# Performance work log

Measured on AMD Instinct MI355X. Metric: run time of the kernel, lower is better.

The kernel has to match this reference:

```python
import jax, jax.numpy as jnp
import numpy as np

N_HIDDEN = 512
BATCH = 16
MAX_LEN = 4096


def setup_inputs() -> dict:
    key = jax.random.key(0)
    k1, k2, k3 = jax.random.split(key, 3)
    h = jax.random.normal(k1, (BATCH, N_HIDDEN, MAX_LEN), dtype=jnp.float32)
    # Conv1d weight [out_ch=3*nh, in_ch=nh, kernel=2], fan-in scaled
    W = jax.random.normal(k2, (3 * N_HIDDEN, N_HIDDEN, 2), dtype=jnp.float32) / np.float32(np.sqrt(2.0 * N_HIDDEN))
    b = 0.02 * jax.random.normal(k3, (3 * N_HIDDEN,), dtype=jnp.float32)
    b = b.at[2 * N_HIDDEN:].set(1.0)  # init_gate_bias on the gate third of the bias
    # lengths: grouped (unique_consecutive) and sorted descending, padded into width MAX_LEN
    N = jnp.array([4096] * 4 + [3000] * 4 + [2048] * 4 + [1000] * 4, dtype=jnp.int32)
    return {"h": h, "W": W, "b": b, "N": N}


def _conv_reduce(h, W, b):
    # _reduce: Conv1d(nh -> 3*nh, kernel=2, stride=2) then gated combine (dropout=0).
    B, C, L = h.shape
    Lp = L + (L % 2)
    x = jnp.pad(h, ((0, 0), (0, 0), (0, Lp - L))).reshape(B, C, Lp // 2, 2)
    lrg = jnp.einsum('bclk,ock->bol', x, W) + b[None, :, None]  # [B, 3C, L//2]
    l = lrg[:, :C]
    r = jnp.tanh(lrg[:, C:2 * C])
    g = jax.nn.sigmoid(lrg[:, 2 * C:])
    return l * g + r * (1.0 - g)


def _forward(h, W, b, N):
    B, nh, L = h.shape
    # Nfp2 = largest power of two <= N ; M = 2*(N - Nfp2)
    Nfp2 = (2 ** jnp.floor(jnp.log2(N.astype(jnp.float32)))).astype(N.dtype)
    M = 2 * (N - Nfp2)
    # --- prefix reduce + suffix cat (padded/masked equivalent of _suffix_cat) ---
    # conv is local (k=2, s=2), so reducing the full padded width gives identical
    # values at the kept positions j < M//2.
    red = _conv_reduce(h, W, b)                      # [B, nh, ceil(L/2)]
    red = jnp.pad(red, ((0, 0), (0, 0), (0, L - red.shape[-1])))
    j = jnp.arange(L)
    half = (M // 2)[:, None]                         # [B, 1]
    take_red = j[None, :] < half                     # first M//2 slots <- reduced prefix
    idx = jnp.where(take_red, j[None, :], jnp.minimum(j[None, :] + half, L - 1))
    suf = jnp.take_along_axis(h, jnp.broadcast_to(idx[:, None, :], (B, nh, L)), axis=2)
    cur = jnp.where(take_red[:, None, :], red, suf)  # per-seq length now Nfp2 (power of 2)
    n = Nfp2
    # --- halving tree reduction; freeze sequences that reached length 1 ---
    steps = int(np.floor(np.log2(L)))
    for _ in range(steps):
        red = _conv_reduce(cur, W, b)
        neww = red.shape[-1]
        active = (n > 1)[:, None, None]
        cur = jnp.where(active, red, cur[:, :, :neww])
        n = jnp.where(n > 1, n // 2, n)
    return cur[:, :, 0]  # squeeze(-1) -> [B, nh]


def reference(h, W, b, N):
    return _forward(h, W, b, N)
```

## Files before the change

### kernel.cpp

```cpp
#include <hip/hip_runtime.h>

#define BATCH 16
#define CH 512
#define OC 1536
#define KDIM 1024
#define LMAX 4096
#define WGLOB_SZ 3145728
#define CTR_OFF 76546048

typedef __attribute__((ext_vector_type(8))) _Float16 h8v;
typedef __attribute__((ext_vector_type(4))) float f4v;

__device__ __forceinline__ int nfp2_of(int n) { return 1 << (31 - __clz(n)); }

__device__ __forceinline__ unsigned short h2u(_Float16 h) {
  union { _Float16 h; unsigned short u; } v; v.h = h; return v.u;
}

__device__ __forceinline__ void layout(const int* __restrict__ Nvec, int b,
                                       size_t& offC0, size_t& offA, size_t& offB,
                                       int& n, int& nfp2, int& half) {
  size_t c0t = 0, at = 0, bt = 0, c0o = 0, ao = 0, bo = 0;
  n = 2; nfp2 = 2; half = 0;
#pragma unroll 1
  for (int i = 0; i < BATCH; ++i) {
    int ni = Nvec[i];
    int f = nfp2_of(ni);
    int hf = ni - f;
    size_t cs = (size_t)((hf + 127) & ~127) << 11;
    size_t as = (size_t)(f >> 1) << 11;
    size_t bs = (size_t)(f >> 2) << 11;
    if (i < b) { c0o += cs; ao += as; bo += bs; }
    if (i == b) { n = ni; nfp2 = f; half = hf; }
    c0t += cs; at += as; bt += bs;
  }
  offC0 = (size_t)WGLOB_SZ + c0o;
  offA = (size_t)WGLOB_SZ + c0t + ao;
  offB = (size_t)WGLOB_SZ + c0t + at + bo;
}

__device__ __forceinline__ void gload16(const void* g, void* l) {
  __builtin_amdgcn_global_load_lds((const __attribute__((address_space(1))) void*)g,
                                   (__attribute__((address_space(3))) void*)l, 16, 0, 0);
}
__device__ __forceinline__ void gload16c(const void* g, void* l) {
  __builtin_amdgcn_global_load_lds((const __attribute__((address_space(1))) void*)g,
                                   (__attribute__((address_space(3))) void*)l, 16, 0, 1);
}

__global__ __launch_bounds__(256) void prep_w_k(const float* __restrict__ W, char* __restrict__ ws) {
  int idx = blockIdx.x * 256 + threadIdx.x;
  if (idx >= 16 * 1536) return;
  int step = idx / 1536;
  int o = idx - step * 1536;
  const float* src = W + (size_t)o * KDIM + step * 64;
  unsigned short hb[64];
#pragma unroll
  for (int t = 0; t < 64; ++t) hb[t] = h2u((_Float16)src[t]);
  uint4* d4 = (uint4*)(ws + ((size_t)idx << 7));
#pragma unroll
  for (int s = 0; s < 8; ++s) {
    int oc = (s ^ (o & 7)) * 8;
    uint4 v;
    v.x = (unsigned)hb[oc + 0] | ((unsigned)hb[oc + 1] << 16);
    v.y = (unsigned)hb[oc + 2] | ((unsigned)hb[oc + 3] << 16);
    v.z = (unsigned)hb[oc + 4] | ((unsigned)hb[oc + 5] << 16);
    v.w = (unsigned)hb[oc + 6] | ((unsigned)hb[oc + 7] << 16);
    d4[s] = v;
  }
}

__global__ void init_ctr_k(char* __restrict__ ws) {
  ((unsigned*)(ws + CTR_OFF))[threadIdx.x] = 0u;
}

__global__ __launch_bounds__(256) void reorg_h_k(const float* __restrict__ h,
                                                 const int* __restrict__ Nvec,
                                                 char* __restrict__ ws,
                                                 float* __restrict__ dout, int mode) {
  __shared__ char T[32 * 256];
  const int b = blockIdx.z;
  size_t offC0, offA, offB; int n, nfp2, half;
  layout(Nvec, b, offC0, offA, offB, n, nfp2, half);
  const int tid = threadIdx.x;
  const int by = blockIdx.y;
  const int c0 = by * 64;

  if (mode == 1 && nfp2 == 1) {
    if (blockIdx.x == 0 && tid < 64)
      dout[(size_t)b * CH + c0 + tid] = h[(size_t)b * CH * LMAX + (size_t)(c0 + tid) * LMAX];
    return;
  }

  const int d0 = blockIdx.x * 32;
  int dlo, dhi, soff;
  size_t base;
  if (mode == 0) { dlo = 0; dhi = half; soff = 0; base = offC0; }
  else { dlo = half >> 1; dhi = nfp2 >> 1; soff = half; base = offA; }
  if (d0 >= dhi || d0 + 32 <= dlo) return;

  const float* hb = h + (size_t)b * CH * LMAX;

#pragma unroll
  for (int q = 0; q < 8; ++q) {
    int id = q * 256 + tid;
    int cl = id >> 5;
    int dl = id & 31;
    int d = d0 + dl;
    bool ok = (d < dhi) && (d >= dlo);
    float2 v;
    v.x = 0.f; v.y = 0.f;
    if (ok) v = *(const float2*)(hb + (size_t)(c0 + cl) * LMAX + 2 * d + soff);
    unsigned u = (unsigned)h2u((_Float16)v.x) | ((unsigned)h2u((_Float16)v.y) << 16);
    int g = cl >> 2;
    *(unsigned*)(T + dl * 256 + ((g ^ (dl & 15)) << 4) + (cl & 3) * 4) = u;
  }
  __syncthreads();
#pragma unroll
  for (int qq = 0; qq < 2; ++qq) {
    int gid = qq * 256 + tid;
    int dl = gid >> 4;
    int s = gid & 15;
    int d = d0 + dl;
    if (d >= dhi || d < dlo) continue;
    uint4 val = *(const uint4*)(T + dl * 256 + ((s ^ (dl & 15)) << 4));
    size_t dst = base + ((size_t)d << 11) + (size_t)((2 * by + (s >> 3)) << 7) +
                 (((s & 7) ^ (d & 7)) << 4);
    *(uint4*)(ws + dst) = val;
  }
}

__device__ __forceinline__ void gate_store(const f4v acc[6][4], const float* __restrict__ bias,
                                           char* outp, float* __restrict__ dout,
                                           int b, int o0, int rg, int cg, int lq, int lane15,
                                           int l0, int cols, bool fin) {
#pragma unroll
  for (int s = 0; s < 2; ++s) {
#pragma unroll
    for (int cf = 0; cf < 4; ++cf) {
      f4v vl = acc[s][cf], vr = acc[2 + s][cf], vg = acc[4 + s][cf];
      int l = l0 + cg * 64 + cf * 16 + lane15;
      if (l >= cols) continue;
      int P = l >> 1, par = l & 1;
#pragma unroll
      for (int j = 0; j < 4; ++j) {
        int c = o0 + rg * 32 + s * 16 + lq * 4 + j;
        float zl = vl[j] + bias[c];
        float zr = vr[j] + bias[CH + c];
        float zg = vg[j] + bias[2 * CH + c];
        float g = 1.f / (1.f + __expf(-zg));
        float rt = 1.f - 2.f / (1.f + __expf(2.f * zr));
        float val = zl * g + rt * (1.f - g);
        if (fin) {
          if (l == 0) dout[(size_t)b * CH + c] = val;
        } else {
          int k = 2 * c + par;
          size_t byte = ((size_t)P << 11) + (size_t)((k >> 6) << 7) +
                        ((((k >> 3) & 7) ^ (P & 7)) << 4) + ((k & 7) << 1);
          *(unsigned short*)(outp + byte) = h2u((_Float16)val);
        }
      }
    }
  }
}

__global__ __launch_bounds__(256, 2) void mfma_level_k(const float* __restrict__ bias,
                                                       const int* __restrict__ Nvec,
                                                       char* __restrict__ ws,
                                                       float* __restrict__ dout,
                                                       int level, int tiles) {
  __shared__ char smem[81920];
  const int id = blockIdx.x;
  const int o0 = (id & 7) * 64;
  const int r2 = id >> 3;
  const int xb = r2 % tiles;
  const int b = r2 / tiles;
  if (b >= BATCH) return;

  size_t offC0, offA, offB; int n, nfp2, half;
  layout(Nvec, b, offC0, offA, offB, n, nfp2, half);

  int cols;
  size_t inOff, outOff;
  if (level == 0) {
    if (half == 0) return;
    cols = half;
    inOff = offC0;
    outOff = offA;
  } else {
    int w = nfp2 >> (level - 1);
    if (w < 2) return;
    cols = w >> 1;
    if (cols <= 128) return;
    inOff = (level & 1) ? offA : offB;
    outOff = (level & 1) ? offB : offA;
  }
  const int l0 = xb * 128;
  if (l0 >= cols) return;

  const int tid = threadIdx.x;
  const int lane = tid & 63, wid = tid >> 6;
  const int lane15 = lane & 15, lq = lane >> 4;
  const int rg = wid & 1, cg = wid >> 1;
  const char* inp = ws + inOff;

  unsigned aoff[6]; int adst[6];
#pragma unroll
  for (int q = 0; q < 6; ++q) {
    int d = q * 4096 + tid * 16;
    int r = d >> 7;
    int p = d & 127;
    int o = ((r >> 6) << 9) + o0 + (r & 63);
    aoff[q] = ((unsigned)o << 7) + p;
    adst[q] = q * 4096 + wid * 1024;
  }
  unsigned boff[4]; int bdst[4];
#pragma unroll
  for (int q = 0; q < 4; ++q) {
    int d = q * 4096 + tid * 16;
    int l = d >> 7;
    int p = d & 127;
    int lc = l0 + l; if (lc > cols - 1) lc = cols - 1;
    boff[q] = ((unsigned)lc << 11) + p;
    bdst[q] = q * 4096 + wid * 1024;
  }

#define STAGE(st, sel) do {                                                  \
    char* Ab = smem + (sel) * 24576;                                         \
    char* Bb = smem + 49152 + (sel) * 16384;                                 \
    unsigned ka = (unsigned)(st) * 196608u;                                  \
    unsigned kb = (unsigned)(st) << 7;                                       \
    _Pragma("unroll") for (int q = 0; q < 6; ++q)                            \
      gload16(ws + ka + aoff[q], Ab + adst[q]);                              \
    _Pragma("unroll") for (int q = 0; q < 4; ++q)                            \
      gload16(inp + kb + boff[q], Bb + bdst[q]);                             \
  } while (0)

  f4v acc[6][4];
#pragma unroll
  for (int m = 0; m < 6; ++m)
#pragma unroll
    for (int cf = 0; cf < 4; ++cf) acc[m][cf] = (f4v){0.f, 0.f, 0.f, 0.f};

  STAGE(0, 0);
  __syncthreads();

#pragma unroll 1
  for (int st = 0; st < 16; ++st) {
    const int cur = st & 1;
    if (st + 1 < 16) STAGE(st + 1, cur ^ 1);
    const char* Asb = smem + cur * 24576;
    const char* Bsb = smem + 49152 + cur * 16384;

#pragma unroll
    for (int s2 = 0; s2 < 2; ++s2) {
      const int oct = (s2 << 2) | lq;
      h8v bh[4];
#pragma unroll
      for (int cf = 0; cf < 4; ++cf) {
        int ll = cg * 64 + cf * 16 + lane15;
        bh[cf] = *(const h8v*)(Bsb + ll * 128 + ((oct ^ (ll & 7)) << 4));
      }
#pragma unroll
      for (int m = 0; m < 6; ++m) {
        int rr = (m >> 1) * 64 + rg * 32 + (m & 1) * 16 + lane15;
        h8v ah = *(const h8v*)(Asb + rr * 128 + ((oct ^ (rr & 7)) << 4));
#pragma unroll
        for (int cf = 0; cf < 4; ++cf)
          acc[m][cf] = __builtin_amdgcn_mfma_f32_16x16x32_f16(ah, bh[cf], acc[m][cf], 0, 0, 0);
      }
    }
    __syncthreads();
  }
#undef STAGE

  bool fin = (level > 0) && ((nfp2 >> level) == 1);
  gate_store(acc, bias, ws + outOff, dout, b, o0, rg, cg, lq, lane15, l0, cols, fin);
}

__global__ __launch_bounds__(256, 2) void tail_k(const float* __restrict__ bias,
                                                 const int* __restrict__ Nvec,
                                                 char* __restrict__ ws,
                                                 float* __restrict__ dout) {
  __shared__ char smem[81920];
  const int id = blockIdx.x;
  const int b = id & 15;
  const int o0 = (id >> 4) * 64;

  size_t offC0, offA, offB; int n, nfp2, half;
  layout(Nvec, b, offC0, offA, offB, n, nfp2, half);
  if (nfp2 < 2) return;

  const int tid = threadIdx.x;
  const int lane = tid & 63, wid = tid >> 6;
  const int lane15 = lane & 15, lq = lane >> 4;
  const int rg = wid & 1, cg = wid >> 1;

  unsigned aoff[6]; int adst[6];
#pragma unroll
  for (int q = 0; q < 6; ++q) {
    int d = q * 4096 + tid * 16;
    int r = d >> 7;
    int p = d & 127;
    int o = ((r >> 6) << 9) + o0 + (r & 63);
    aoff[q] = ((unsigned)o << 7) + p;
    adst[q] = q * 4096 + wid * 1024;
  }

  unsigned* ctr = (unsigned*)(ws + CTR_OFF) + b * 16;

  int lev = 1;
  while ((nfp2 >> lev) > 128) ++lev;

#pragma unroll 1
  for (;; ++lev) {
    int w = nfp2 >> (lev - 1);
    if (w < 2) break;
    const int cols = nfp2 >> lev;
    const bool fin = (cols == 1);
    const char* inp = ws + ((lev & 1) ? offA : offB);
    char* outp = ws + ((lev & 1) ? offB : offA);

    unsigned boff[4]; int bdst[4];
#pragma unroll
    for (int q = 0; q < 4; ++q) {
      int d = q * 4096 + tid * 16;
      int l = d >> 7;
      int p = d & 127;
      int lc = l; if (lc > cols - 1) lc = cols - 1;
      boff[q] = ((unsigned)lc << 11) + p;
      bdst[q] = q * 4096 + wid * 1024;
    }

#define STAGE_T(st, sel) do {                                                \
    char* Ab = smem + (sel) * 24576;                                         \
    char* Bb = smem + 49152 + (sel) * 16384;                                 \
    unsigned ka = (unsigned)(st) * 196608u;                                  \
    unsigned kb = (unsigned)(st) << 7;                                       \
    _Pragma("unroll") for (int q = 0; q < 6; ++q)                            \
      gload16(ws + ka + aoff[q], Ab + adst[q]);                              \
    _Pragma("unroll") for (int q = 0; q < 4; ++q)                            \
      gload16c(inp + kb + boff[q], Bb + bdst[q]);                            \
  } while (0)

    f4v acc[6][4];
#pragma unroll
    for (int m = 0; m < 6; ++m)
#pragma unroll
      for (int cf = 0; cf < 4; ++cf) acc[m][cf] = (f4v){0.f, 0.f, 0.f, 0.f};

    STAGE_T(0, 0);
    __syncthreads();

#pragma unroll 1
    for (int st = 0; st < 16; ++st) {
      const int cur = st & 1;
      if (st + 1 < 16) STAGE_T(st + 1, cur ^ 1);
      const char* Asb = smem + cur * 24576;
      const char* Bsb = smem + 49152 + cur * 16384;

#pragma unroll
      for (int s2 = 0; s2 < 2; ++s2) {
        const int oct = (s2 << 2) | lq;
        h8v bh[4];
#pragma unroll
        for (int cf = 0; cf < 4; ++cf) {
          int ll = cg * 64 + cf * 16 + lane15;
          bh[cf] = *(const h8v*)(Bsb + ll * 128 + ((oct ^ (ll & 7)) << 4));
        }
#pragma unroll
        for (int m = 0; m < 6; ++m) {
          int rr = (m >> 1) * 64 + rg * 32 + (m & 1) * 16 + lane15;
          h8v ah = *(const h8v*)(Asb + rr * 128 + ((oct ^ (rr & 7)) << 4));
#pragma unroll
          for (int cf = 0; cf < 4; ++cf)
            acc[m][cf] = __builtin_amdgcn_mfma_f32_16x16x32_f16(ah, bh[cf], acc[m][cf], 0, 0, 0);
        }
      }
      __syncthreads();
    }
#undef STAGE_T

    gate_store(acc, bias, outp, dout, b, o0, rg, cg, lq, lane15, 0, cols, fin);
    if (fin) break;

    __threadfence();
    __syncthreads();
    if (tid == 0) {
      atomicAdd(ctr + lev, 1u);
      while (atomicAdd(ctr + lev, 0u) < 8u) __builtin_amdgcn_s_sleep(8);
    }
    __syncthreads();
  }
}

extern "C" void kernel_launch(void* const* d_in, const int* in_sizes, int n_in,
                              void* d_out, int out_size, void* d_ws, size_t ws_size,
                              hipStream_t stream) {
  const float* h = (const float*)d_in[0];
  const float* W = (const float*)d_in[1];
  const float* bias = (const float*)d_in[2];
  const int* Nvec = (const int*)d_in[3];
  float* dout = (float*)d_out;
  char* ws = (char*)d_ws;

  prep_w_k<<<dim3(96), 256, 0, stream>>>(W, ws);
  init_ctr_k<<<dim3(1), 256, 0, stream>>>(ws);
  reorg_h_k<<<dim3(64, 8, BATCH), 256, 0, stream>>>(h, Nvec, ws, dout, 0);
  reorg_h_k<<<dim3(64, 8, BATCH), 256, 0, stream>>>(h, Nvec, ws, dout, 1);

  mfma_level_k<<<dim3(8 * 8 * BATCH), 256, 0, stream>>>(bias, Nvec, ws, dout, 0, 8);
  for (int lev = 1; lev <= 4; ++lev) {
    int tiles = (LMAX >> lev) / 128;
    mfma_level_k<<<dim3(tiles * 8 * BATCH), 256, 0, stream>>>(bias, Nvec, ws, dout, lev, tiles);
  }
  tail_k<<<dim3(128), 256, 0, stream>>>(bias, Nvec, ws, dout);
}
```

Measured before the change: 527.3 us.

## Widen level GEMM tiles and pipeline A/B loads with triple buffering

```diff
diff --git a/kernel.cpp b/kernel.cpp
--- a/kernel.cpp
+++ b/kernel.cpp
@@ -164,12 +164,12 @@
   }
 }
 
-__global__ __launch_bounds__(256, 2) void mfma_level_k(const float* __restrict__ bias,
+__global__ __launch_bounds__(512, 2) void mfma_level_k(const float* __restrict__ bias,
                                                        const int* __restrict__ Nvec,
                                                        char* __restrict__ ws,
                                                        float* __restrict__ dout,
                                                        int level, int tiles) {
-  __shared__ char smem[81920];
+  __shared__ char smem[139264];
   const int id = blockIdx.x;
   const int o0 = (id & 7) * 64;
   const int r2 = id >> 3;
@@ -195,7 +195,7 @@
     inOff = (level & 1) ? offA : offB;
     outOff = (level & 1) ? offB : offA;
   }
-  const int l0 = xb * 128;
+  const int l0 = xb * 256;
   if (l0 >= cols) return;
 
   const int tid = threadIdx.x;
@@ -204,34 +204,36 @@
   const int rg = wid & 1, cg = wid >> 1;
   const char* inp = ws + inOff;
 
-  unsigned aoff[6]; int adst[6];
-#pragma unroll
-  for (int q = 0; q < 6; ++q) {
-    int d = q * 4096 + tid * 16;
+  unsigned aoff[3]; int adst[3];
+#pragma unroll
+  for (int q = 0; q < 3; ++q) {
+    int d = q * 8192 + tid * 16;
     int r = d >> 7;
     int p = d & 127;
     int o = ((r >> 6) << 9) + o0 + (r & 63);
     aoff[q] = ((unsigned)o << 7) + p;
-    adst[q] = q * 4096 + wid * 1024;
+    adst[q] = q * 8192 + wid * 1024;
   }
   unsigned boff[4]; int bdst[4];
 #pragma unroll
   for (int q = 0; q < 4; ++q) {
-    int d = q * 4096 + tid * 16;
+    int d = q * 8192 + tid * 16;
     int l = d >> 7;
     int p = d & 127;
     int lc = l0 + l; if (lc > cols - 1) lc = cols - 1;
     boff[q] = ((unsigned)lc << 11) + p;
-    bdst[q] = q * 4096 + wid * 1024;
-  }
-
-#define STAGE(st, sel) do {                                                  \
+    bdst[q] = q * 8192 + wid * 1024;
+  }
+
+#define STAGE_A(st, sel) do {                                                \
     char* Ab = smem + (sel) * 24576;                                         \
-    char* Bb = smem + 49152 + (sel) * 16384;                                 \
     unsigned ka = (unsigned)(st) * 196608u;                                  \
+    _Pragma("unroll") for (int q = 0; q < 3; ++q)                            \
+      gload16(ws + ka + aoff[q], Ab + adst[q]);                              \
+  } while (0)
+#define STAGE_B(st, sel) do {                                                \
+    char* Bb = smem + 73728 + (sel) * 32768;                                 \
     unsigned kb = (unsigned)(st) << 7;                                       \
-    _Pragma("unroll") for (int q = 0; q < 6; ++q)                            \
-      gload16(ws + ka + aoff[q], Ab + adst[q]);                              \
     _Pragma("unroll") for (int q = 0; q < 4; ++q)                            \
       gload16(inp + kb + boff[q], Bb + bdst[q]);                             \
   } while (0)
@@ -242,15 +244,22 @@
 #pragma unroll
     for (int cf = 0; cf < 4; ++cf) acc[m][cf] = (f4v){0.f, 0.f, 0.f, 0.f};
 
-  STAGE(0, 0);
-  __syncthreads();
-
+  STAGE_A(0, 0);
+  STAGE_B(0, 0);
+  STAGE_A(1, 1);
+
+  int acur = 0, anx2 = 2;
 #pragma unroll 1
   for (int st = 0; st < 16; ++st) {
-    const int cur = st & 1;
-    if (st + 1 < 16) STAGE(st + 1, cur ^ 1);
-    const char* Asb = smem + cur * 24576;
-    const char* Bsb = smem + 49152 + cur * 16384;
+    if (st < 15) asm volatile("s_waitcnt vmcnt(3) lgkmcnt(0)" ::: "memory");
+    else         asm volatile("s_waitcnt vmcnt(0) lgkmcnt(0)" ::: "memory");
+    __builtin_amdgcn_s_barrier();
+    asm volatile("" ::: "memory");
+    if (st + 1 < 16) STAGE_B(st + 1, (st + 1) & 1);
+    if (st + 2 < 16) STAGE_A(st + 2, anx2);
+
+    const char* Asb = smem + acur * 24576;
+    const char* Bsb = smem + 73728 + (st & 1) * 32768;
 
 #pragma unroll
     for (int s2 = 0; s2 < 2; ++s2) {
@@ -261,6 +270,7 @@
         int ll = cg * 64 + cf * 16 + lane15;
         bh[cf] = *(const h8v*)(Bsb + ll * 128 + ((oct ^ (ll & 7)) << 4));
       }
+      __builtin_amdgcn_s_setprio(1);
 #pragma unroll
       for (int m = 0; m < 6; ++m) {
         int rr = (m >> 1) * 64 + rg * 32 + (m & 1) * 16 + lane15;
@@ -269,10 +279,13 @@
         for (int cf = 0; cf < 4; ++cf)
           acc[m][cf] = __builtin_amdgcn_mfma_f32_16x16x32_f16(ah, bh[cf], acc[m][cf], 0, 0, 0);
       }
+      __builtin_amdgcn_s_setprio(0);
     }
-    __syncthreads();
-  }
-#undef STAGE
+    acur = (acur == 2) ? 0 : acur + 1;
+    anx2 = (anx2 == 2) ? 0 : anx2 + 1;
+  }
+#undef STAGE_A
+#undef STAGE_B
 
   bool fin = (level > 0) && ((nfp2 >> level) == 1);
   gate_store(acc, bias, ws + outOff, dout, b, o0, rg, cg, lq, lane15, l0, cols, fin);
@@ -282,7 +295,7 @@
                                                  const int* __restrict__ Nvec,
                                                  char* __restrict__ ws,
                                                  float* __restrict__ dout) {
-  __shared__ char smem[81920];
+  __shared__ char smem[106496];
   const int id = blockIdx.x;
   const int b = id & 15;
   const int o0 = (id >> 4) * 64;
@@ -332,13 +345,15 @@
       bdst[q] = q * 4096 + wid * 1024;
     }
 
-#define STAGE_T(st, sel) do {                                                \
+#define STAGE_AT(st, sel) do {                                               \
     char* Ab = smem + (sel) * 24576;                                         \
-    char* Bb = smem + 49152 + (sel) * 16384;                                 \
     unsigned ka = (unsigned)(st) * 196608u;                                  \
-    unsigned kb = (unsigned)(st) << 7;                                       \
     _Pragma("unroll") for (int q = 0; q < 6; ++q)                            \
       gload16(ws + ka + aoff[q], Ab + adst[q]);                              \
+  } while (0)
+#define STAGE_BT(st, sel) do {                                               \
+    char* Bb = smem + 73728 + (sel) * 16384;                                 \
+    unsigned kb = (unsigned)(st) << 7;                                       \
     _Pragma("unroll") for (int q = 0; q < 4; ++q)                            \
       gload16c(inp + kb + boff[q], Bb + bdst[q]);                            \
   } while (0)
@@ -349,15 +364,22 @@
 #pragma unroll
       for (int cf = 0; cf < 4; ++cf) acc[m][cf] = (f4v){0.f, 0.f, 0.f, 0.f};
 
-    STAGE_T(0, 0);
-    __syncthreads();
-
+    STAGE_AT(0, 0);
+    STAGE_BT(0, 0);
+    STAGE_AT(1, 1);
+
+    int acur = 0, anx2 = 2;
 #pragma unroll 1
     for (int st = 0; st < 16; ++st) {
-      const int cur = st & 1;
-      if (st + 1 < 16) STAGE_T(st + 1, cur ^ 1);
-      const char* Asb = smem + cur * 24576;
-      const char* Bsb = smem + 49152 + cur * 16384;
+      if (st < 15) asm volatile("s_waitcnt vmcnt(6) lgkmcnt(0)" ::: "memory");
+      else         asm volatile("s_waitcnt vmcnt(0) lgkmcnt(0)" ::: "memory");
+      __builtin_amdgcn_s_barrier();
+      asm volatile("" ::: "memory");
+      if (st + 1 < 16) STAGE_BT(st + 1, (st + 1) & 1);
+      if (st + 2 < 16) STAGE_AT(st + 2, anx2);
+
+      const char* Asb = smem + acur * 24576;
+      const char* Bsb = smem + 73728 + (st & 1) * 16384;
 
 #pragma unroll
       for (int s2 = 0; s2 < 2; ++s2) {
@@ -377,9 +399,11 @@
             acc[m][cf] = __builtin_amdgcn_mfma_f32_16x16x32_f16(ah, bh[cf], acc[m][cf], 0, 0, 0);
         }
       }
-      __syncthreads();
+      acur = (acur == 2) ? 0 : acur + 1;
+      anx2 = (anx2 == 2) ? 0 : anx2 + 1;
     }
-#undef STAGE_T
+#undef STAGE_AT
+#undef STAGE_BT
 
     gate_store(acc, bias, outp, dout, b, o0, rg, cg, lq, lane15, 0, cols, fin);
     if (fin) break;
@@ -409,10 +433,10 @@
   reorg_h_k<<<dim3(64, 8, BATCH), 256, 0, stream>>>(h, Nvec, ws, dout, 0);
   reorg_h_k<<<dim3(64, 8, BATCH), 256, 0, stream>>>(h, Nvec, ws, dout, 1);
 
-  mfma_level_k<<<dim3(8 * 8 * BATCH), 256, 0, stream>>>(bias, Nvec, ws, dout, 0, 8);
+  mfma_level_k<<<dim3(4 * 8 * BATCH), 512, 0, stream>>>(bias, Nvec, ws, dout, 0, 4);
   for (int lev = 1; lev <= 4; ++lev) {
-    int tiles = (LMAX >> lev) / 128;
-    mfma_level_k<<<dim3(tiles * 8 * BATCH), 256, 0, stream>>>(bias, Nvec, ws, dout, lev, tiles);
+    int tiles = (LMAX >> lev) / 256; if (tiles < 1) tiles = 1;
+    mfma_level_k<<<dim3(tiles * 8 * BATCH), 512, 0, stream>>>(bias, Nvec, ws, dout, lev, tiles);
   }
   tail_k<<<dim3(128), 256, 0, stream>>>(bias, Nvec, ws, dout);
 }
```

New measurement: 573.0 us. +8.7%, slower.
